# Performance work log

Measured on AMD Instinct MI355X. Metric: run time of the kernel, lower is better.

## Reference

```python
import jax, jax.numpy as jnp
import numpy as np

DIM = 192
HEADS = 6
WS = 7
N = WS * WS  # 49
B_ = 4096
NW = 64


def _relative_position_index(ws):
    coords = np.stack(np.meshgrid(np.arange(ws), np.arange(ws), indexing='ij'))  # (2, ws, ws)
    cf = coords.reshape(2, -1)  # (2, N)
    rel = cf[:, :, None] - cf[:, None, :]  # (2, N, N)
    rel = rel.transpose(1, 2, 0).copy()
    rel[:, :, 0] += ws - 1
    rel[:, :, 1] += ws - 1
    rel[:, :, 0] *= 2 * ws - 1
    return jnp.asarray(rel.sum(-1), dtype=jnp.int32)  # (N, N)


def setup_inputs() -> dict:
    key = jax.random.key(0)
    ks = jax.random.split(key, 8)
    x = jax.random.normal(ks[0], (B_, N, DIM), dtype=jnp.float32)
    mask = jax.random.normal(ks[1], (NW, N, N), dtype=jnp.float32)
    qkv_w = jax.random.normal(ks[2], (3 * DIM, DIM), dtype=jnp.float32) * 0.02
    qkv_b = jnp.zeros((3 * DIM,), dtype=jnp.float32)
    proj_w = jax.random.normal(ks[3], (DIM, DIM), dtype=jnp.float32) * 0.02
    proj_b = jnp.zeros((DIM,), dtype=jnp.float32)
    n_bias = (2 * WS - 1) * (2 * WS - 1)  # 169
    bias_table = jax.random.truncated_normal(ks[4], -2.0, 2.0, (n_bias, HEADS), dtype=jnp.float32) * 0.02
    rel_idx = _relative_position_index(WS)
    return {"x": x, "mask": mask, "qkv_w": qkv_w, "qkv_b": qkv_b,
            "proj_w": proj_w, "proj_b": proj_b, "bias_table": bias_table,
            "rel_idx": rel_idx}


def reference(x, mask, qkv_w, qkv_b, proj_w, proj_b, bias_table, rel_idx):
    Bw, n, c = x.shape
    hd = c // HEADS
    scale = hd ** -0.5
    qkv = x @ qkv_w.T + qkv_b  # (B_, N, 3C)
    qkv = qkv.reshape(Bw, n, 3, HEADS, hd).transpose(2, 0, 3, 1, 4)  # (3, B_, H, N, hd)
    q, k, v = qkv[0] * scale, qkv[1], qkv[2]
    attn = jnp.einsum('bhqd,bhkd->bhqk', q, k)  # (B_, H, N, N)
    bias = bias_table[rel_idx.reshape(-1)].reshape(n, n, HEADS).transpose(2, 0, 1)  # (H, N, N)
    attn = attn + bias[None]
    nW = mask.shape[0]
    attn = attn.reshape(Bw // nW, nW, HEADS, n, n) + mask[None, :, None]
    attn = jax.nn.softmax(attn.reshape(Bw, HEADS, n, n), axis=-1)
    out = jnp.einsum('bhqk,bhkd->bhqd', attn, v)  # (B_, H, N, hd)
    out = out.transpose(0, 2, 1, 3).reshape(Bw, n, c)
    return out @ proj_w.T + proj_b
```

## Files before the change

kernel.cpp:

```cpp
#include <hip/hip_runtime.h>
#include <hip/hip_fp16.h>


typedef short bf16x8 __attribute__((ext_vector_type(8)));
typedef float f32x4 __attribute__((ext_vector_type(4)));

#define MFMA16(a, b, c) __builtin_amdgcn_mfma_f32_16x16x32_bf16((a), (b), (c), 0, 0, 0)

#define DIMC 192
#define NTOK 49

__device__ __forceinline__ unsigned short f2bf(float f) {
  unsigned int u = __float_as_uint(f);
  u += 0x7fffu + ((u >> 16) & 1u);
  return (unsigned short)(u >> 16);
}

__global__ void prep_kernel(const float* __restrict__ qkv_w,
                            const float* __restrict__ proj_w,
                            const float* __restrict__ bias_table,
                            const int* __restrict__ rel_idx,
                            unsigned short* __restrict__ qkv_wb,
                            unsigned short* __restrict__ proj_wb,
                            float* __restrict__ biasP) {
  int i = blockIdx.x * 256 + threadIdx.x;
  if (i < 576 * 192) qkv_wb[i] = f2bf(qkv_w[i]);
  if (i < 192 * 192) proj_wb[i] = f2bf(proj_w[i]);
  if (i < 6 * 64 * 64) {
    int h = i >> 12;
    int rr = i & 4095;
    int r = rr >> 6, c = rr & 63;
    float v = 0.f;
    if (r < NTOK && c < NTOK) v = bias_table[rel_idx[r * NTOK + c] * 6 + h];
    biasP[i] = v;
  }
}

__global__ __launch_bounds__(256, 2) void winattn_kernel(
    const float* __restrict__ x,
    const float* __restrict__ mask,
    const float* __restrict__ qkv_b,
    const float* __restrict__ proj_b,
    const unsigned short* __restrict__ qkv_wb,
    const unsigned short* __restrict__ proj_wb,
    const float* __restrict__ biasP,
    float* __restrict__ out) {
  __shared__ unsigned short xb[64 * 200];
  __shared__ unsigned short Qs[64 * 40];
  __shared__ unsigned short Ks[64 * 40];
  __shared__ unsigned short Vts[32 * 72];
  __shared__ unsigned short Pb[4 * 16 * 72];
  __shared__ unsigned short Ob[64 * 40];
  __shared__ __half maskS[64 * 64];

  const int tid = threadIdx.x;
  const int b = blockIdx.x;
  const int widx = b & 63;
  const int lane = tid & 63;
  const int wv = tid >> 6;
  const int lq = lane >> 4;
  const int ln = lane & 15;

  {
    const float4* xp = (const float4*)(x + (size_t)b * (NTOK * DIMC));
    for (int i = tid; i < NTOK * DIMC / 4; i += 256) {
      float4 v = xp[i];
      int fl = i * 4;
      int r = fl / DIMC;
      int c = fl - r * DIMC;
      unsigned int lo = (unsigned int)f2bf(v.x) | ((unsigned int)f2bf(v.y) << 16);
      unsigned int hi = (unsigned int)f2bf(v.z) | ((unsigned int)f2bf(v.w) << 16);
      *(uint2*)(&xb[r * 200 + c]) = make_uint2(lo, hi);
    }
    for (int i = tid; i < 15 * 200 / 2; i += 256)
      ((unsigned int*)(&xb[49 * 200]))[i] = 0u;
    const float* mp = mask + (size_t)widx * (NTOK * NTOK);
    for (int i = tid; i < 64 * 64; i += 256) {
      int r = i >> 6, c = i & 63;
      float v = (c >= NTOK) ? -30000.f : ((r >= NTOK) ? 0.f : mp[r * NTOK + c]);
      maskS[i] = __float2half(v);
    }
  }

  f32x4 pacc[4][3];
  for (int nti = 0; nti < 3; ++nti) {
    float pbv = proj_b[(wv * 3 + nti) * 16 + ln];
    for (int mt = 0; mt < 4; ++mt) pacc[mt][nti] = (f32x4){pbv, pbv, pbv, pbv};
  }
  __syncthreads();

  const float scale = 0.17677669529663687f;

  for (int h = 0; h < 6; ++h) {
    for (int tt = 0; tt < 6; tt += 2) {
      int t0 = wv * 6 + tt;
      int t1 = t0 + 1;
      int nt0 = t0 >> 2, mt0 = t0 & 3;
      int nt1 = t1 >> 2, mt1 = t1 & 3;
      int oc0 = (nt0 >> 1) * DIMC + h * 32 + (nt0 & 1) * 16 + ln;
      int oc1 = (nt1 >> 1) * DIMC + h * 32 + (nt1 & 1) * 16 + ln;
      const unsigned short* w0p = qkv_wb + (size_t)oc0 * DIMC + lq * 8;
      const unsigned short* w1p = qkv_wb + (size_t)oc1 * DIMC + lq * 8;
      bf16x8 w0[6], w1[6];
      for (int ks = 0; ks < 6; ++ks) {
        w0[ks] = *(const bf16x8*)(w0p + ks * 32);
        w1[ks] = *(const bf16x8*)(w1p + ks * 32);
      }
      float b0 = qkv_b[oc0], b1 = qkv_b[oc1];
      f32x4 acc0 = (f32x4){b0, b0, b0, b0};
      f32x4 acc1 = (f32x4){b1, b1, b1, b1};
      const unsigned short* a0p = &xb[(mt0 * 16 + ln) * 200 + lq * 8];
      const unsigned short* a1p = &xb[(mt1 * 16 + ln) * 200 + lq * 8];
      for (int ks = 0; ks < 6; ++ks) {
        bf16x8 a0 = *(const bf16x8*)(a0p + ks * 32);
        bf16x8 a1 = *(const bf16x8*)(a1p + ks * 32);
        acc0 = MFMA16(a0, w0[ks], acc0);
        acc1 = MFMA16(a1, w1[ks], acc1);
      }
      {
        int which = nt0 >> 1, db = (nt0 & 1) * 16 + ln, row0 = mt0 * 16 + lq * 4;
        if (which == 0) {
          for (int r = 0; r < 4; ++r) Qs[(row0 + r) * 40 + db] = f2bf(acc0[r] * scale);
        } else if (which == 1) {
          for (int r = 0; r < 4; ++r) Ks[(row0 + r) * 40 + db] = f2bf(acc0[r]);
        } else {
          unsigned int lo = (unsigned int)f2bf(acc0[0]) | ((unsigned int)f2bf(acc0[1]) << 16);
          unsigned int hi = (unsigned int)f2bf(acc0[2]) | ((unsigned int)f2bf(acc0[3]) << 16);
          *(uint2*)(&Vts[db * 72 + row0]) = make_uint2(lo, hi);
        }
      }
      {
        int which = nt1 >> 1, db = (nt1 & 1) * 16 + ln, row0 = mt1 * 16 + lq * 4;
        if (which == 0) {
          for (int r = 0; r < 4; ++r) Qs[(row0 + r) * 40 + db] = f2bf(acc1[r] * scale);
        } else if (which == 1) {
          for (int r = 0; r < 4; ++r) Ks[(row0 + r) * 40 + db] = f2bf(acc1[r]);
        } else {
          unsigned int lo = (unsigned int)f2bf(acc1[0]) | ((unsigned int)f2bf(acc1[1]) << 16);
          unsigned int hi = (unsigned int)f2bf(acc1[2]) | ((unsigned int)f2bf(acc1[3]) << 16);
          *(uint2*)(&Vts[db * 72 + row0]) = make_uint2(lo, hi);
        }
      }
    }
    __syncthreads();

    {
      const int mt = wv;
      bf16x8 kf[4], vf0[2], vf1[2];
      for (int nt = 0; nt < 4; ++nt)
        kf[nt] = *(const bf16x8*)&Ks[(nt * 16 + ln) * 40 + lq * 8];
      for (int nv = 0; nv < 2; ++nv) {
        vf0[nv] = *(const bf16x8*)&Vts[(nv * 16 + ln) * 72 + lq * 8];
        vf1[nv] = *(const bf16x8*)&Vts[(nv * 16 + ln) * 72 + 32 + lq * 8];
      }
      bf16x8 qf = *(const bf16x8*)&Qs[(mt * 16 + ln) * 40 + lq * 8];
      f32x4 sv[4];
      for (int nt = 0; nt < 4; ++nt)
        sv[nt] = MFMA16(qf, kf[nt], ((f32x4){0.f, 0.f, 0.f, 0.f}));

      int row0 = mt * 16 + lq * 4;
      const float* bp = biasP + ((size_t)h * 64 + row0) * 64;
      float tt[4][4];
      for (int nt = 0; nt < 4; ++nt) {
        int col = nt * 16 + ln;
        for (int r = 0; r < 4; ++r)
          tt[nt][r] = sv[nt][r] + bp[r * 64 + col] + __half2float(maskS[(row0 + r) * 64 + col]);
      }
      float pinv[4];
      for (int r = 0; r < 4; ++r) {
        float m = fmaxf(fmaxf(tt[0][r], tt[1][r]), fmaxf(tt[2][r], tt[3][r]));
        m = fmaxf(m, __shfl_xor(m, 1, 64));
        m = fmaxf(m, __shfl_xor(m, 2, 64));
        m = fmaxf(m, __shfl_xor(m, 4, 64));
        m = fmaxf(m, __shfl_xor(m, 8, 64));
        float sum = 0.f;
        for (int nt = 0; nt < 4; ++nt) {
          float e = __expf(tt[nt][r] - m);
          tt[nt][r] = e;
          sum += e;
        }
        sum += __shfl_xor(sum, 1, 64);
        sum += __shfl_xor(sum, 2, 64);
        sum += __shfl_xor(sum, 4, 64);
        sum += __shfl_xor(sum, 8, 64);
        pinv[r] = 1.f / sum;
      }
      unsigned short* Pw = &Pb[wv * 16 * 72];
      for (int nt = 0; nt < 4; ++nt) {
        int col = nt * 16 + ln;
        for (int r = 0; r < 4; ++r) Pw[(lq * 4 + r) * 72 + col] = f2bf(tt[nt][r]);
      }
      bf16x8 pa0 = *(const bf16x8*)&Pw[ln * 72 + lq * 8];
      bf16x8 pa1 = *(const bf16x8*)&Pw[ln * 72 + 32 + lq * 8];
      f32x4 o0 = (f32x4){0.f, 0.f, 0.f, 0.f};
      f32x4 o1 = (f32x4){0.f, 0.f, 0.f, 0.f};
      o0 = MFMA16(pa0, vf0[0], o0);
      o0 = MFMA16(pa1, vf1[0], o0);
      o1 = MFMA16(pa0, vf0[1], o1);
      o1 = MFMA16(pa1, vf1[1], o1);
      for (int r = 0; r < 4; ++r) {
        int row = row0 + r;
        Ob[row * 40 + ln] = f2bf(o0[r] * pinv[r]);
        Ob[row * 40 + 16 + ln] = f2bf(o1[r] * pinv[r]);
      }
    }
    __syncthreads();

    {
      bf16x8 oa[4];
      for (int mt = 0; mt < 4; ++mt)
        oa[mt] = *(const bf16x8*)&Ob[(mt * 16 + ln) * 40 + lq * 8];
      for (int nti = 0; nti < 3; ++nti) {
        int o = (wv * 3 + nti) * 16 + ln;
        bf16x8 w = *(const bf16x8*)(proj_wb + (size_t)o * DIMC + h * 32 + lq * 8);
        for (int mt = 0; mt < 4; ++mt)
          pacc[mt][nti] = MFMA16(oa[mt], w, pacc[mt][nti]);
      }
    }
    __syncthreads();
  }

  {
    float* outp = out + (size_t)b * (NTOK * DIMC);
    for (int nti = 0; nti < 3; ++nti) {
      int col = (wv * 3 + nti) * 16 + ln;
      for (int mt = 0; mt < 4; ++mt) {
        int row0 = mt * 16 + lq * 4;
        for (int r = 0; r < 4; ++r) {
          int row = row0 + r;
          if (row < NTOK) outp[row * DIMC + col] = pacc[mt][nti][r];
        }
      }
    }
  }
}

extern "C" void kernel_launch(void* const* d_in, const int* in_sizes, int n_in,
                              void* d_out, int out_size, void* d_ws, size_t ws_size,
                              hipStream_t stream) {
  const float* x = (const float*)d_in[0];
  const float* mask = (const float*)d_in[1];
  const float* qkv_w = (const float*)d_in[2];
  const float* qkv_b = (const float*)d_in[3];
  const float* proj_w = (const float*)d_in[4];
  const float* proj_b = (const float*)d_in[5];
  const float* bias_table = (const float*)d_in[6];
  const int* rel_idx = (const int*)d_in[7];

  unsigned short* qkv_wb = (unsigned short*)d_ws;
  unsigned short* proj_wb = qkv_wb + 576 * 192;
  float* biasP = (float*)(proj_wb + 192 * 192);

  prep_kernel<<<432, 256, 0, stream>>>(qkv_w, proj_w, bias_table, rel_idx,
                                       qkv_wb, proj_wb, biasP);
  winattn_kernel<<<4096, 256, 0, stream>>>(x, mask, qkv_b, proj_b,
                                           qkv_wb, proj_wb, biasP,
                                           (float*)d_out);
}
```

Measured before the change: 613.5 us.

## Keep attention probabilities in registers, precombine bias+mask, raise occupancy

```diff
diff --git a/kernel.cpp b/kernel.cpp
--- a/kernel.cpp
+++ b/kernel.cpp
@@ -16,42 +16,53 @@
   return (unsigned short)(u >> 16);
 }
 
+__device__ __forceinline__ unsigned int cvt_pk_bf16(float lo, float hi) {
+  unsigned int r;
+  asm("v_cvt_pk_bf16_f32 %0, %1, %2" : "=v"(r) : "v"(lo), "v"(hi));
+  return r;
+}
+
 __global__ void prep_kernel(const float* __restrict__ qkv_w,
                             const float* __restrict__ proj_w,
                             const float* __restrict__ bias_table,
                             const int* __restrict__ rel_idx,
+                            const float* __restrict__ mask,
                             unsigned short* __restrict__ qkv_wb,
                             unsigned short* __restrict__ proj_wb,
-                            float* __restrict__ biasP) {
+                            __half* __restrict__ bmT) {
   int i = blockIdx.x * 256 + threadIdx.x;
   if (i < 576 * 192) qkv_wb[i] = f2bf(qkv_w[i]);
   if (i < 192 * 192) proj_wb[i] = f2bf(proj_w[i]);
-  if (i < 6 * 64 * 64) {
-    int h = i >> 12;
-    int rr = i & 4095;
-    int r = rr >> 6, c = rr & 63;
-    float v = 0.f;
-    if (r < NTOK && c < NTOK) v = bias_table[rel_idx[r * NTOK + c] * 6 + h];
-    biasP[i] = v;
-  }
-}
-
-__global__ __launch_bounds__(256, 2) void winattn_kernel(
+  {
+    int r = i & 3;
+    int q = (i >> 2) & 63;
+    int lq = (i >> 8) & 3;
+    int nt = (i >> 10) & 3;
+    int hw = i >> 12;
+    int h = hw % 6;
+    int widx = hw / 6;
+    int k = nt * 16 + lq * 4 + r;
+    float v;
+    if (k >= NTOK) v = -30000.f;
+    else if (q >= NTOK) v = 0.f;
+    else v = bias_table[rel_idx[q * NTOK + k] * 6 + h] +
+             mask[(size_t)widx * (NTOK * NTOK) + q * NTOK + k];
+    bmT[i] = __float2half(v);
+  }
+}
+
+__global__ __launch_bounds__(256, 4) void winattn_kernel(
     const float* __restrict__ x,
-    const float* __restrict__ mask,
     const float* __restrict__ qkv_b,
     const float* __restrict__ proj_b,
     const unsigned short* __restrict__ qkv_wb,
     const unsigned short* __restrict__ proj_wb,
-    const float* __restrict__ biasP,
+    const __half* __restrict__ bmT,
     float* __restrict__ out) {
   __shared__ unsigned short xb[64 * 200];
   __shared__ unsigned short Qs[64 * 40];
   __shared__ unsigned short Ks[64 * 40];
   __shared__ unsigned short Vts[32 * 72];
-  __shared__ unsigned short Pb[4 * 16 * 72];
-  __shared__ unsigned short Ob[64 * 40];
-  __shared__ __half maskS[64 * 64];
 
   const int tid = threadIdx.x;
   const int b = blockIdx.x;
@@ -74,24 +85,31 @@
     }
     for (int i = tid; i < 15 * 200 / 2; i += 256)
       ((unsigned int*)(&xb[49 * 200]))[i] = 0u;
-    const float* mp = mask + (size_t)widx * (NTOK * NTOK);
-    for (int i = tid; i < 64 * 64; i += 256) {
-      int r = i >> 6, c = i & 63;
-      float v = (c >= NTOK) ? -30000.f : ((r >= NTOK) ? 0.f : mp[r * NTOK + c]);
-      maskS[i] = __float2half(v);
-    }
-  }
-
-  f32x4 pacc[4][3];
-  for (int nti = 0; nti < 3; ++nti) {
-    float pbv = proj_b[(wv * 3 + nti) * 16 + ln];
-    for (int mt = 0; mt < 4; ++mt) pacc[mt][nti] = (f32x4){pbv, pbv, pbv, pbv};
+  }
+
+  f32x4 pacc[12];
+#pragma unroll
+  for (int nti = 0; nti < 12; ++nti) {
+    float pbv = proj_b[nti * 16 + ln];
+    pacc[nti] = (f32x4){pbv, pbv, pbv, pbv};
   }
   __syncthreads();
 
   const float scale = 0.17677669529663687f;
+  const __half* bmp = bmT + (size_t)widx * 6 * 4096;
+  const int sA = ((lq & 1) << 5) | ln;
+  const int sB = sA + 16;
+  const int hiSel = lq >> 1;
 
   for (int h = 0; h < 6; ++h) {
+    uint2 bmu[4];
+    {
+      const __half* bmh = bmp + (size_t)h * 4096;
+#pragma unroll
+      for (int nt = 0; nt < 4; ++nt)
+        bmu[nt] = *(const uint2*)(bmh + ((nt * 4 + lq) * 64 + wv * 16 + ln) * 4);
+    }
+
     for (int tt = 0; tt < 6; tt += 2) {
       int t0 = wv * 6 + tt;
       int t1 = t0 + 1;
@@ -102,6 +120,7 @@
       const unsigned short* w0p = qkv_wb + (size_t)oc0 * DIMC + lq * 8;
       const unsigned short* w1p = qkv_wb + (size_t)oc1 * DIMC + lq * 8;
       bf16x8 w0[6], w1[6];
+#pragma unroll
       for (int ks = 0; ks < 6; ++ks) {
         w0[ks] = *(const bf16x8*)(w0p + ks * 32);
         w1[ks] = *(const bf16x8*)(w1p + ks * 32);
@@ -111,6 +130,7 @@
       f32x4 acc1 = (f32x4){b1, b1, b1, b1};
       const unsigned short* a0p = &xb[(mt0 * 16 + ln) * 200 + lq * 8];
       const unsigned short* a1p = &xb[(mt1 * 16 + ln) * 200 + lq * 8];
+#pragma unroll
       for (int ks = 0; ks < 6; ++ks) {
         bf16x8 a0 = *(const bf16x8*)(a0p + ks * 32);
         bf16x8 a1 = *(const bf16x8*)(a1p + ks * 32);
@@ -120,24 +140,28 @@
       {
         int which = nt0 >> 1, db = (nt0 & 1) * 16 + ln, row0 = mt0 * 16 + lq * 4;
         if (which == 0) {
+#pragma unroll
           for (int r = 0; r < 4; ++r) Qs[(row0 + r) * 40 + db] = f2bf(acc0[r] * scale);
         } else if (which == 1) {
+#pragma unroll
           for (int r = 0; r < 4; ++r) Ks[(row0 + r) * 40 + db] = f2bf(acc0[r]);
         } else {
-          unsigned int lo = (unsigned int)f2bf(acc0[0]) | ((unsigned int)f2bf(acc0[1]) << 16);
-          unsigned int hi = (unsigned int)f2bf(acc0[2]) | ((unsigned int)f2bf(acc0[3]) << 16);
+          unsigned int lo = cvt_pk_bf16(acc0[0], acc0[1]);
+          unsigned int hi = cvt_pk_bf16(acc0[2], acc0[3]);
           *(uint2*)(&Vts[db * 72 + row0]) = make_uint2(lo, hi);
         }
       }
       {
         int which = nt1 >> 1, db = (nt1 & 1) * 16 + ln, row0 = mt1 * 16 + lq * 4;
         if (which == 0) {
+#pragma unroll
           for (int r = 0; r < 4; ++r) Qs[(row0 + r) * 40 + db] = f2bf(acc1[r] * scale);
         } else if (which == 1) {
+#pragma unroll
           for (int r = 0; r < 4; ++r) Ks[(row0 + r) * 40 + db] = f2bf(acc1[r]);
         } else {
-          unsigned int lo = (unsigned int)f2bf(acc1[0]) | ((unsigned int)f2bf(acc1[1]) << 16);
-          unsigned int hi = (unsigned int)f2bf(acc1[2]) | ((unsigned int)f2bf(acc1[3]) << 16);
+          unsigned int lo = cvt_pk_bf16(acc1[0], acc1[1]);
+          unsigned int hi = cvt_pk_bf16(acc1[2], acc1[3]);
           *(uint2*)(&Vts[db * 72 + row0]) = make_uint2(lo, hi);
         }
       }
@@ -145,76 +169,89 @@
     __syncthreads();
 
     {
-      const int mt = wv;
-      bf16x8 kf[4], vf0[2], vf1[2];
+      bf16x8 qf = *(const bf16x8*)&Qs[(wv * 16 + ln) * 40 + lq * 8];
+      f32x4 sv[4];
+#pragma unroll
+      for (int nt = 0; nt < 4; ++nt) {
+        bf16x8 kf = *(const bf16x8*)&Ks[(nt * 16 + ln) * 40 + lq * 8];
+        sv[nt] = MFMA16(kf, qf, ((f32x4){0.f, 0.f, 0.f, 0.f}));
+      }
+      float tt[4][4];
+#pragma unroll
+      for (int nt = 0; nt < 4; ++nt) {
+        float2 f01 = __half22float2(*(const __half2*)&bmu[nt].x);
+        float2 f23 = __half22float2(*(const __half2*)&bmu[nt].y);
+        tt[nt][0] = sv[nt][0] + f01.x;
+        tt[nt][1] = sv[nt][1] + f01.y;
+        tt[nt][2] = sv[nt][2] + f23.x;
+        tt[nt][3] = sv[nt][3] + f23.y;
+      }
+      float m = tt[0][0];
+#pragma unroll
       for (int nt = 0; nt < 4; ++nt)
-        kf[nt] = *(const bf16x8*)&Ks[(nt * 16 + ln) * 40 + lq * 8];
-      for (int nv = 0; nv < 2; ++nv) {
-        vf0[nv] = *(const bf16x8*)&Vts[(nv * 16 + ln) * 72 + lq * 8];
-        vf1[nv] = *(const bf16x8*)&Vts[(nv * 16 + ln) * 72 + 32 + lq * 8];
-      }
-      bf16x8 qf = *(const bf16x8*)&Qs[(mt * 16 + ln) * 40 + lq * 8];
-      f32x4 sv[4];
+#pragma unroll
+        for (int r = 0; r < 4; ++r) m = fmaxf(m, tt[nt][r]);
+      m = fmaxf(m, __shfl_xor(m, 16, 64));
+      m = fmaxf(m, __shfl_xor(m, 32, 64));
+      float sum = 0.f;
+#pragma unroll
       for (int nt = 0; nt < 4; ++nt)
-        sv[nt] = MFMA16(qf, kf[nt], ((f32x4){0.f, 0.f, 0.f, 0.f}));
-
-      int row0 = mt * 16 + lq * 4;
-      const float* bp = biasP + ((size_t)h * 64 + row0) * 64;
-      float tt[4][4];
-      for (int nt = 0; nt < 4; ++nt) {
-        int col = nt * 16 + ln;
-        for (int r = 0; r < 4; ++r)
-          tt[nt][r] = sv[nt][r] + bp[r * 64 + col] + __half2float(maskS[(row0 + r) * 64 + col]);
-      }
-      float pinv[4];
-      for (int r = 0; r < 4; ++r) {
-        float m = fmaxf(fmaxf(tt[0][r], tt[1][r]), fmaxf(tt[2][r], tt[3][r]));
-        m = fmaxf(m, __shfl_xor(m, 1, 64));
-        m = fmaxf(m, __shfl_xor(m, 2, 64));
-        m = fmaxf(m, __shfl_xor(m, 4, 64));
-        m = fmaxf(m, __shfl_xor(m, 8, 64));
-        float sum = 0.f;
-        for (int nt = 0; nt < 4; ++nt) {
+#pragma unroll
+        for (int r = 0; r < 4; ++r) {
           float e = __expf(tt[nt][r] - m);
           tt[nt][r] = e;
           sum += e;
         }
-        sum += __shfl_xor(sum, 1, 64);
-        sum += __shfl_xor(sum, 2, 64);
-        sum += __shfl_xor(sum, 4, 64);
-        sum += __shfl_xor(sum, 8, 64);
-        pinv[r] = 1.f / sum;
-      }
-      unsigned short* Pw = &Pb[wv * 16 * 72];
+      sum += __shfl_xor(sum, 16, 64);
+      sum += __shfl_xor(sum, 32, 64);
+      float pinv = 1.f / sum;
+
+      unsigned int pk[4][2];
+#pragma unroll
       for (int nt = 0; nt < 4; ++nt) {
-        int col = nt * 16 + ln;
-        for (int r = 0; r < 4; ++r) Pw[(lq * 4 + r) * 72 + col] = f2bf(tt[nt][r]);
-      }
-      bf16x8 pa0 = *(const bf16x8*)&Pw[ln * 72 + lq * 8];
-      bf16x8 pa1 = *(const bf16x8*)&Pw[ln * 72 + 32 + lq * 8];
-      f32x4 o0 = (f32x4){0.f, 0.f, 0.f, 0.f};
-      f32x4 o1 = (f32x4){0.f, 0.f, 0.f, 0.f};
-      o0 = MFMA16(pa0, vf0[0], o0);
-      o0 = MFMA16(pa1, vf1[0], o0);
-      o1 = MFMA16(pa0, vf0[1], o1);
-      o1 = MFMA16(pa1, vf1[1], o1);
-      for (int r = 0; r < 4; ++r) {
-        int row = row0 + r;
-        Ob[row * 40 + ln] = f2bf(o0[r] * pinv[r]);
-        Ob[row * 40 + 16 + ln] = f2bf(o1[r] * pinv[r]);
-      }
-    }
-    __syncthreads();
-
-    {
-      bf16x8 oa[4];
-      for (int mt = 0; mt < 4; ++mt)
-        oa[mt] = *(const bf16x8*)&Ob[(mt * 16 + ln) * 40 + lq * 8];
-      for (int nti = 0; nti < 3; ++nti) {
-        int o = (wv * 3 + nti) * 16 + ln;
-        bf16x8 w = *(const bf16x8*)(proj_wb + (size_t)o * DIMC + h * 32 + lq * 8);
-        for (int mt = 0; mt < 4; ++mt)
-          pacc[mt][nti] = MFMA16(oa[mt], w, pacc[mt][nti]);
+        pk[nt][0] = cvt_pk_bf16(tt[nt][0], tt[nt][1]);
+        pk[nt][1] = cvt_pk_bf16(tt[nt][2], tt[nt][3]);
+      }
+      union U8 { unsigned int u[4]; bf16x8 v; };
+      U8 pb0, pb1;
+#pragma unroll
+      for (int w = 0; w < 4; ++w) {
+        int src = (w & 2) ? sB : sA;
+        int a0 = __shfl((int)pk[0][w & 1], src, 64);
+        int a1 = __shfl((int)pk[1][w & 1], src, 64);
+        int b0 = __shfl((int)pk[2][w & 1], src, 64);
+        int b1 = __shfl((int)pk[3][w & 1], src, 64);
+        pb0.u[w] = (unsigned int)(hiSel ? a1 : a0);
+        pb1.u[w] = (unsigned int)(hiSel ? b1 : b0);
+      }
+      f32x4 o[2];
+#pragma unroll
+      for (int db = 0; db < 2; ++db) {
+        bf16x8 v0 = *(const bf16x8*)&Vts[(db * 16 + ln) * 72 + lq * 8];
+        bf16x8 v1 = *(const bf16x8*)&Vts[(db * 16 + ln) * 72 + 32 + lq * 8];
+        f32x4 acc = (f32x4){0.f, 0.f, 0.f, 0.f};
+        acc = MFMA16(v0, pb0.v, acc);
+        acc = MFMA16(v1, pb1.v, acc);
+        o[db] = acc;
+      }
+      unsigned int pkO[2][2];
+#pragma unroll
+      for (int db = 0; db < 2; ++db) {
+        pkO[db][0] = cvt_pk_bf16(o[db][0] * pinv, o[db][1] * pinv);
+        pkO[db][1] = cvt_pk_bf16(o[db][2] * pinv, o[db][3] * pinv);
+      }
+      U8 oa;
+#pragma unroll
+      for (int w = 0; w < 4; ++w) {
+        int src = (w & 2) ? sB : sA;
+        int a0 = __shfl((int)pkO[0][w & 1], src, 64);
+        int a1 = __shfl((int)pkO[1][w & 1], src, 64);
+        oa.u[w] = (unsigned int)(hiSel ? a1 : a0);
+      }
+#pragma unroll
+      for (int nti = 0; nti < 12; ++nti) {
+        bf16x8 w = *(const bf16x8*)(proj_wb + (size_t)(nti * 16 + ln) * DIMC + h * 32 + lq * 8);
+        pacc[nti] = MFMA16(oa.v, w, pacc[nti]);
       }
     }
     __syncthreads();
@@ -222,14 +259,13 @@
 
   {
     float* outp = out + (size_t)b * (NTOK * DIMC);
-    for (int nti = 0; nti < 3; ++nti) {
-      int col = (wv * 3 + nti) * 16 + ln;
-      for (int mt = 0; mt < 4; ++mt) {
-        int row0 = mt * 16 + lq * 4;
-        for (int r = 0; r < 4; ++r) {
-          int row = row0 + r;
-          if (row < NTOK) outp[row * DIMC + col] = pacc[mt][nti][r];
-        }
+#pragma unroll
+    for (int nti = 0; nti < 12; ++nti) {
+      int col = nti * 16 + ln;
+#pragma unroll
+      for (int r = 0; r < 4; ++r) {
+        int row = wv * 16 + lq * 4 + r;
+        if (row < NTOK) outp[row * DIMC + col] = pacc[nti][r];
       }
     }
   }
@@ -249,11 +285,11 @@
 
   unsigned short* qkv_wb = (unsigned short*)d_ws;
   unsigned short* proj_wb = qkv_wb + 576 * 192;
-  float* biasP = (float*)(proj_wb + 192 * 192);
-
-  prep_kernel<<<432, 256, 0, stream>>>(qkv_w, proj_w, bias_table, rel_idx,
-                                       qkv_wb, proj_wb, biasP);
-  winattn_kernel<<<4096, 256, 0, stream>>>(x, mask, qkv_b, proj_b,
-                                           qkv_wb, proj_wb, biasP,
+  __half* bmT = (__half*)(proj_wb + 192 * 192);
+
+  prep_kernel<<<6144, 256, 0, stream>>>(qkv_w, proj_w, bias_table, rel_idx,
+                                        mask, qkv_wb, proj_wb, bmT);
+  winattn_kernel<<<4096, 256, 0, stream>>>(x, qkv_b, proj_b,
+                                           qkv_wb, proj_wb, bmT,
                                            (float*)d_out);
 }
```

New measurement: 627.5 us. 1.02x slower.
